# Optimization experiments

Hardware: AMD Instinct MI355X
Metric: run time of the kernel (lower is better)

## Reference

```python
import jax, jax.numpy as jnp
import numpy as np

S, F, H, A, B = 11, 650, 1024, 47, 4096
NEG = -1e9  # stand-in for -inf in masked_fill; softmax weight becomes exactly 0 numerically


def _layernorm(x, g, b):
    m = x.mean(-1, keepdims=True)
    v = ((x - m) ** 2).mean(-1, keepdims=True)
    return (x - m) / jnp.sqrt(v + 1e-5) * g + b


def setup_inputs() -> dict:
    key = jax.random.key(0)
    ks = jax.random.split(key, 16)

    def lin(k, fan_in, fan_out):
        kw, kb = jax.random.split(k)
        s = 1.0 / np.sqrt(fan_in)
        W = jax.random.uniform(kw, (fan_in, fan_out), minval=-s, maxval=s, dtype=jnp.float32)
        b = jax.random.uniform(kb, (fan_out,), minval=-s, maxval=s, dtype=jnp.float32)
        return W, b

    obs = jax.random.normal(ks[0], (B, S, F), dtype=jnp.float32)
    action_mask = jax.random.randint(ks[1], (B, 2, A), 0, 2).astype(jnp.int32)
    action_mask = action_mask.at[:, :, :8].set(1)  # guarantee legal actions per row
    u = jax.random.uniform(ks[2], (B, 2, A), minval=1e-6, maxval=1.0)
    gumbel = -jnp.log(-jnp.log(u))

    W0, b0 = lin(ks[3], S * F, H)
    W1, b1 = lin(ks[4], H, H)
    W2, b2 = lin(ks[5], H, H)
    Wp, bp = lin(ks[6], H, 2 * A)
    Wv, bv = lin(ks[7], H, 1)
    ones = jnp.ones((H,), jnp.float32)
    zeros = jnp.zeros((H,), jnp.float32)
    return {
        'obs': obs, 'action_mask': action_mask, 'gumbel': gumbel,
        'W0': W0, 'b0': b0, 'g0': ones, 'be0': zeros,
        'W1': W1, 'b1': b1, 'g1': ones, 'be1': zeros,
        'W2': W2, 'b2': b2, 'g2': ones, 'be2': zeros,
        'Wp': Wp, 'bp': bp, 'Wv': Wv, 'bv': bv,
    }


def _forward(obs, action_mask, gumbel, W0, b0, g0, be0, W1, b1, g1, be1, W2, b2, g2, be2, Wp, bp, Wv, bv):
    x = obs.reshape(obs.shape[0], -1)
    x = jax.nn.relu(_layernorm(x @ W0 + b0, g0, be0))
    x = jax.nn.relu(_layernorm(x @ W1 + b1, g1, be1))
    x = jax.nn.relu(_layernorm(x @ W2 + b2, g2, be2))  # dropout = eval-mode identity
    policy_logits = (x @ Wp + bp).reshape(-1, 2, A)
    value = (x @ Wv + bv)[:, 0]

    bsz = policy_logits.shape[0]
    rows = jnp.arange(bsz)
    ar = jnp.arange(A)

    # head 1: masked categorical via Gumbel-max
    l1 = jnp.where(action_mask[:, 0, :] == 0, NEG, policy_logits[:, 0, :])
    a1 = jnp.argmax(l1 + gumbel[:, 0, :], axis=-1)
    logp1 = jax.nn.log_softmax(l1, axis=-1)[rows, a1]

    # vectorized mutual-exclusivity mask update (replaces per-batch Python loop)
    m2 = action_mask[:, 1, :]
    oh = ar[None, :] == a1[:, None]
    c_switch = (a1 >= 1) & (a1 <= 6)
    m2 = jnp.where(c_switch[:, None] & oh, 0, m2)
    c_tera = (a1 > 26) & (a1 <= 46)
    rng = (ar >= 27) & (ar < 47)
    m2 = jnp.where(c_tera[:, None] & rng[None, :], 0, m2)
    c_zero = a1 == 0
    col0 = (ar == 0)[None, :]
    m2 = jnp.where(c_zero[:, None] & col0, 0, m2)
    empty = (m2.sum(-1) == 0) & c_zero
    m2 = jnp.where(empty[:, None] & col0, 1, m2)

    l2 = jnp.where(m2 == 0, NEG, policy_logits[:, 1, :])
    a2 = jnp.argmax(l2 + gumbel[:, 1, :], axis=-1)
    logp2 = jax.nn.log_softmax(l2, axis=-1)[rows, a2]

    sampled_actions = jnp.stack([a1, a2], axis=-1)
    policy_log_probs = jnp.stack([logp1, logp2], axis=-1)
    return policy_logits, policy_log_probs, sampled_actions, value


def reference(obs, action_mask, gumbel, W0, b0, g0, be0, W1, b1, g1, be1, W2, b2, g2, be2, Wp, bp, Wv, bv):
    return _forward(obs, action_mask, gumbel, W0, b0, g0, be0, W1, b1, g1, be1, W2, b2, g2, be2, Wp, bp, Wv, bv)
```

## Files before the change

kernel.cpp:

```cpp
#include <hip/hip_runtime.h>
#include <math.h>

#define BATCH 4096
#define HDIM  1024
#define KDIM0 7150
#define KP0   7168
#define KT0   224
#define KTH   32
#define NACT  47
#define NA2   94
#define NEGC  -1000000000.0f

#define LP_OFF  385024
#define ACT_OFF 393216
#define VAL_OFF 401408

typedef _Float16 half8_t  __attribute__((ext_vector_type(8)));
typedef _Float16 half4_t  __attribute__((ext_vector_type(4)));
typedef float    float4_t __attribute__((ext_vector_type(4)));

#define GLOAD16(gp, lp) __builtin_amdgcn_global_load_lds( \
    (__attribute__((address_space(1))) void*)(gp), \
    (__attribute__((address_space(3))) void*)(lp), 16, 0, 0)


__global__ __launch_bounds__(256) void wconv_frag_kernel(
    const float* __restrict__ W, _Float16* __restrict__ Wh,
    _Float16* __restrict__ Wl, int K, int KT)
{
  __shared__ float T[64][65];
  const int k0 = blockIdx.x * 64, n0 = blockIdx.y * 64, t = threadIdx.x;
#pragma unroll
  for (int p = 0; p < 16; ++p) {
    const int idx = p * 256 + t;
    const int r = idx >> 6, c = idx & 63;
    T[r][c] = (k0 + r < K) ? W[(size_t)(k0 + r) * HDIM + n0 + c] : 0.f;
  }
  __syncthreads();
#pragma unroll
  for (int ss = 0; ss < 2; ++ss) {
    const int s    = ss * 256 + t;
    const int tile = s >> 6;
    const int ktl  = tile >> 2, ntl = tile & 3;
    const int lane = s & 63;
    const int quad = lane >> 4, nr = lane & 15;
    half8_t h, l;
#pragma unroll
    for (int j = 0; j < 8; ++j) {
      const float v = T[ktl * 32 + quad * 8 + j][ntl * 16 + nr];
      const _Float16 hh = (_Float16)v;
      h[j] = hh;
      l[j] = (_Float16)((v - (float)hh) * 4096.f);
    }
    const size_t o = ((size_t)((n0 / 16 + ntl) * KT + (k0 / 32 + ktl)) * 64 + lane) * 8;
    *(half8_t*)(Wh + o) = h;
    *(half8_t*)(Wl + o) = l;
  }
}

__global__ __launch_bounds__(512, 4) void gemm_obs_kernel(
    const float* __restrict__ A,
    const _Float16* __restrict__ Wh, const _Float16* __restrict__ Wl,
    float* __restrict__ C, int ktsplit)
{
  __shared__ _Float16 As[2][2][8][512];
  __shared__ _Float16 Ws[2][2][8][512];
  const int f  = blockIdx.x + 8 * (blockIdx.y + 32 * blockIdx.z);
  const int nf = (f & 7) * 64 + (f >> 3);
  const int bx = nf & 7, by = (nf >> 3) & 31, bz = nf >> 8;

  const int t    = threadIdx.x;
  const int lane = t & 63;
  const int w    = t >> 6;
  const int nt0  = bx * 8;
  const int mt0  = by * 8;
  const int ktb  = bz * ktsplit;
  const int nit  = ktsplit;
  const int l15  = lane & 15, quad = lane >> 4;
  const int wmi  = (w >> 2) * 4;
  const int wni  = (w & 3) * 2;

  const float* aRow = A + (size_t)((mt0 + w) * 16 + l15) * KDIM0 + quad * 8;
  const _Float16* wS0 = Wh + (size_t)(nt0 + w) * KT0 * 512 + lane * 8;
  const _Float16* wS1 = Wl + (size_t)(nt0 + w) * KT0 * 512 + lane * 8;

  struct AF8 { float v[8]; };
  auto loadA = [&](int kt) {
    AF8 r;
    const int kg = kt * 32 + quad * 8;
    const float* src = aRow + (size_t)kt * 32;
    if (kg + 8 <= KDIM0) {
#pragma unroll
      for (int c = 0; c < 4; ++c) {
        const float2 p = *(const float2*)(src + c * 2);
        r.v[c * 2] = p.x; r.v[c * 2 + 1] = p.y;
      }
    } else {
#pragma unroll
      for (int j = 0; j < 8; ++j)
        r.v[j] = (kg + j < KDIM0) ? src[j] : 0.f;
    }
    return r;
  };
  auto gw = [&](int kt, int buf) {
    GLOAD16(wS0 + (size_t)kt * 512, &Ws[buf][0][w][0]);
    GLOAD16(wS1 + (size_t)kt * 512, &Ws[buf][1][w][0]);
  };
  auto convst = [&](const AF8& a, int buf) {
    half8_t h, l;
#pragma unroll
    for (int j = 0; j < 8; ++j) {
      const float v = a.v[j];
      const _Float16 hh = (_Float16)v;
      h[j] = hh;
      l[j] = (_Float16)((v - (float)hh) * 4096.f);
    }
    *(half8_t*)&As[buf][0][w][lane * 8] = h;
    *(half8_t*)&As[buf][1][w][lane * 8] = l;
  };

  float4_t acc[4][2], accx[4][2];
#pragma unroll
  for (int i = 0; i < 4; ++i)
#pragma unroll
    for (int j = 0; j < 2; ++j) {
      acc[i][j]  = (float4_t){0.f, 0.f, 0.f, 0.f};
      accx[i][j] = (float4_t){0.f, 0.f, 0.f, 0.f};
    }

  auto mm = [&](int buf) {
    half8_t ah[4], al[4], wh[2], wl[2];
#pragma unroll
    for (int i = 0; i < 4; ++i) {
      ah[i] = *(const half8_t*)&As[buf][0][wmi + i][lane * 8];
      al[i] = *(const half8_t*)&As[buf][1][wmi + i][lane * 8];
    }
#pragma unroll
    for (int j = 0; j < 2; ++j) {
      wh[j] = *(const half8_t*)&Ws[buf][0][wni + j][lane * 8];
      wl[j] = *(const half8_t*)&Ws[buf][1][wni + j][lane * 8];
    }
#pragma unroll
    for (int i = 0; i < 4; ++i)
#pragma unroll
      for (int j = 0; j < 2; ++j) {
        acc[i][j]  = __builtin_amdgcn_mfma_f32_16x16x32_f16(ah[i], wh[j], acc[i][j], 0, 0, 0);
        accx[i][j] = __builtin_amdgcn_mfma_f32_16x16x32_f16(ah[i], wl[j], accx[i][j], 0, 0, 0);
        accx[i][j] = __builtin_amdgcn_mfma_f32_16x16x32_f16(al[i], wh[j], accx[i][j], 0, 0, 0);
      }
  };

  AF8 vaE = loadA(ktb + 0);
  AF8 vaO = loadA(ktb + 1);
  gw(ktb + 0, 0);
  convst(vaE, 0);
  __syncthreads();

  for (int it = 0; it < nit; it += 2) {
    gw(ktb + it + 1, 1);
    convst(vaO, 1);
    if (it + 2 < nit) vaE = loadA(ktb + it + 2);
    mm(0);
    __syncthreads();
    if (it + 2 < nit) { gw(ktb + it + 2, 0); convst(vaE, 0); }
    if (it + 3 < nit) vaO = loadA(ktb + it + 3);
    mm(1);
    __syncthreads();
  }

  float* Cb = C + (size_t)bz * ((size_t)BATCH * HDIM);
  const float sc = 1.0f / 4096.0f;
#pragma unroll
  for (int i = 0; i < 4; ++i) {
    const int row0 = (mt0 + wmi + i) * 16 + quad * 4;
#pragma unroll
    for (int j = 0; j < 2; ++j) {
      const int col = (nt0 + wni + j) * 16 + l15;
      float* cp = Cb + (size_t)row0 * HDIM + col;
#pragma unroll
      for (int r = 0; r < 4; ++r)
        cp[(size_t)r * HDIM] = acc[i][j][r] + accx[i][j][r] * sc;
    }
  }
}

__global__ __launch_bounds__(512, 4) void gemm_frag2_kernel(
    const _Float16* __restrict__ Ah, const _Float16* __restrict__ Al,
    const _Float16* __restrict__ Wh, const _Float16* __restrict__ Wl,
    float* __restrict__ C, int KT, int ktsplit)
{
  __shared__ _Float16 As[2][2][8][512];
  __shared__ _Float16 Ws[2][2][8][512];
  const int f  = blockIdx.x + 8 * (blockIdx.y + 32 * blockIdx.z);
  const int nf = (f & 7) * 64 + (f >> 3);
  const int bx = nf & 7, by = (nf >> 3) & 31, bz = nf >> 8;

  const int t    = threadIdx.x;
  const int lane = t & 63;
  const int w    = t >> 6;
  const int nt0  = bx * 8;
  const int mt0  = by * 8;
  const int ktb  = bz * ktsplit;
  const int nit  = ktsplit;
  const int l15  = lane & 15, quad = lane >> 4;
  const int wmi  = (w >> 2) * 4;
  const int wni  = (w & 3) * 2;

  const _Float16* aS0 = Ah + (size_t)(mt0 + w) * KT * 512 + lane * 8;
  const _Float16* aS1 = Al + (size_t)(mt0 + w) * KT * 512 + lane * 8;
  const _Float16* wS0 = Wh + (size_t)(nt0 + w) * KT * 512 + lane * 8;
  const _Float16* wS1 = Wl + (size_t)(nt0 + w) * KT * 512 + lane * 8;

  auto st = [&](int kt, int buf) {
    GLOAD16(aS0 + (size_t)kt * 512, &As[buf][0][w][0]);
    GLOAD16(aS1 + (size_t)kt * 512, &As[buf][1][w][0]);
    GLOAD16(wS0 + (size_t)kt * 512, &Ws[buf][0][w][0]);
    GLOAD16(wS1 + (size_t)kt * 512, &Ws[buf][1][w][0]);
  };

  float4_t acc[4][2], accx[4][2];
#pragma unroll
  for (int i = 0; i < 4; ++i)
#pragma unroll
    for (int j = 0; j < 2; ++j) {
      acc[i][j]  = (float4_t){0.f, 0.f, 0.f, 0.f};
      accx[i][j] = (float4_t){0.f, 0.f, 0.f, 0.f};
    }

  auto mm = [&](int buf) {
    half8_t ah[4], al[4], wh[2], wl[2];
#pragma unroll
    for (int i = 0; i < 4; ++i) {
      ah[i] = *(const half8_t*)&As[buf][0][wmi + i][lane * 8];
      al[i] = *(const half8_t*)&As[buf][1][wmi + i][lane * 8];
    }
#pragma unroll
    for (int j = 0; j < 2; ++j) {
      wh[j] = *(const half8_t*)&Ws[buf][0][wni + j][lane * 8];
      wl[j] = *(const half8_t*)&Ws[buf][1][wni + j][lane * 8];
    }
#pragma unroll
    for (int i = 0; i < 4; ++i)
#pragma unroll
      for (int j = 0; j < 2; ++j) {
        acc[i][j]  = __builtin_amdgcn_mfma_f32_16x16x32_f16(ah[i], wh[j], acc[i][j], 0, 0, 0);
        accx[i][j] = __builtin_amdgcn_mfma_f32_16x16x32_f16(ah[i], wl[j], accx[i][j], 0, 0, 0);
        accx[i][j] = __builtin_amdgcn_mfma_f32_16x16x32_f16(al[i], wh[j], accx[i][j], 0, 0, 0);
      }
  };

  st(ktb, 0);
  __syncthreads();
  for (int it = 0; it < nit; it += 2) {
    st(ktb + it + 1, 1);
    mm(0);
    __syncthreads();
    if (it + 2 < nit) st(ktb + it + 2, 0);
    mm(1);
    __syncthreads();
  }

  float* Cb = C + (size_t)bz * ((size_t)BATCH * HDIM);
  const float sc = 1.0f / 4096.0f;
#pragma unroll
  for (int i = 0; i < 4; ++i) {
    const int row0 = (mt0 + wmi + i) * 16 + quad * 4;
#pragma unroll
    for (int j = 0; j < 2; ++j) {
      const int col = (nt0 + wni + j) * 16 + l15;
      float* cp = Cb + (size_t)row0 * HDIM + col;
#pragma unroll
      for (int r = 0; r < 4; ++r)
        cp[(size_t)r * HDIM] = acc[i][j][r] + accx[i][j][r] * sc;
    }
  }
}

__global__ __launch_bounds__(1024) void ln_relu_f16_frag_kernel(
    const float* __restrict__ x0, const float* __restrict__ x1,
    const float* __restrict__ bias,
    const float* __restrict__ g, const float* __restrict__ be,
    _Float16* __restrict__ oh, _Float16* __restrict__ ol)
{
  const int t = threadIdx.x;
  const int w = t >> 6, lane = t & 63;
  const int mt = blockIdx.x;
  const float* xr0 = x0 + (size_t)(mt * 16 + w) * HDIM;
  const float* xr1 = x1 + (size_t)(mt * 16 + w) * HDIM;

  float4 v[4];
  float s = 0.f;
#pragma unroll
  for (int c = 0; c < 4; ++c) {
    const int k = c * 256 + lane * 4;
    const float4 a = *(const float4*)(xr0 + k);
    const float4 b = *(const float4*)(xr1 + k);
    const float4 bb = *(const float4*)(bias + k);
    v[c].x = a.x + b.x + bb.x; v[c].y = a.y + b.y + bb.y;
    v[c].z = a.z + b.z + bb.z; v[c].w = a.w + b.w + bb.w;
    s += (v[c].x + v[c].y) + (v[c].z + v[c].w);
  }
#pragma unroll
  for (int o = 32; o; o >>= 1) s += __shfl_xor(s, o, 64);
  const float mean = s * (1.0f / HDIM);

  float s2 = 0.f;
#pragma unroll
  for (int c = 0; c < 4; ++c) {
    v[c].x -= mean; v[c].y -= mean; v[c].z -= mean; v[c].w -= mean;
    s2 += (v[c].x * v[c].x + v[c].y * v[c].y) + (v[c].z * v[c].z + v[c].w * v[c].w);
  }
#pragma unroll
  for (int o = 32; o; o >>= 1) s2 += __shfl_xor(s2, o, 64);
  const float inv = 1.0f / sqrtf(s2 * (1.0f / HDIM) + 1e-5f);

  const int kt_b  = lane >> 3;
  const int quad  = (lane >> 1) & 3;
  const int jb    = (lane & 1) * 4;
#pragma unroll
  for (int c = 0; c < 4; ++c) {
    const int k = c * 256 + lane * 4;
    const float4 gg = *(const float4*)(g + k);
    const float4 ee = *(const float4*)(be + k);
    float r0 = fmaxf(fmaf(v[c].x * inv, gg.x, ee.x), 0.f);
    float r1 = fmaxf(fmaf(v[c].y * inv, gg.y, ee.y), 0.f);
    float r2 = fmaxf(fmaf(v[c].z * inv, gg.z, ee.z), 0.f);
    float r3 = fmaxf(fmaf(v[c].w * inv, gg.w, ee.w), 0.f);
    const _Float16 h0 = (_Float16)r0, h1 = (_Float16)r1, h2 = (_Float16)r2, h3 = (_Float16)r3;
    const half4_t hv = {h0, h1, h2, h3};
    const half4_t lv = {(_Float16)((r0 - (float)h0) * 4096.f),
                        (_Float16)((r1 - (float)h1) * 4096.f),
                        (_Float16)((r2 - (float)h2) * 4096.f),
                        (_Float16)((r3 - (float)h3) * 4096.f)};
    const int kt = c * 8 + kt_b;
    const size_t o = ((size_t)(mt * KTH + kt) * 64 + quad * 16 + w) * 8 + jb;
    *(half4_t*)(oh + o) = hv;
    *(half4_t*)(ol + o) = lv;
  }
}

__global__ __launch_bounds__(256) void pack_wcat_kernel(
    const float* __restrict__ Wp, const float* __restrict__ Wv,
    float* __restrict__ Wc)
{
  const int i = blockIdx.x * 256 + threadIdx.x;
  const int k = i / 96, c = i % 96;
  float v = 0.f;
  if (c < 94)       v = Wp[(size_t)k * 94 + c];
  else if (c == 94) v = Wv[k];
  Wc[i] = v;
}

__global__ __launch_bounds__(256) void head_fused_kernel(
    const float* __restrict__ x0, const float* __restrict__ x1,
    const float* __restrict__ b2, const float* __restrict__ g2,
    const float* __restrict__ be2,
    const float* __restrict__ Wc, const float* __restrict__ bp,
    const float* __restrict__ bv,
    const int* __restrict__ amask, const float* __restrict__ gum,
    float* __restrict__ out)
{
  __shared__ float Xs[8][1025];
  __shared__ float red[4][8][96];
  __shared__ float fl[8][96];
  __shared__ float rstat[16];
  const int t  = threadIdx.x;
  const int r0 = blockIdx.x * 8;
  const int wv = t >> 6, lane = t & 63;

#pragma unroll 4
  for (int i = 0; i < 32; ++i) {
    const int e = i * 256 + t;
    const int r = e >> 10, k = e & 1023;
    const size_t gi = (size_t)(r0 + r) * HDIM + k;
    Xs[r][k] = x0[gi] + x1[gi] + b2[k];
  }
  __syncthreads();

#pragma unroll
  for (int rr = 0; rr < 2; ++rr) {
    const int row = wv + rr * 4;
    float s = 0.f;
#pragma unroll
    for (int ii = 0; ii < 16; ++ii) s += Xs[row][lane + 64 * ii];
#pragma unroll
    for (int o = 32; o; o >>= 1) s += __shfl_xor(s, o, 64);
    const float mean = s * (1.0f / HDIM);
    float s2 = 0.f;
#pragma unroll
    for (int ii = 0; ii < 16; ++ii) {
      const float d = Xs[row][lane + 64 * ii] - mean;
      s2 += d * d;
    }
#pragma unroll
    for (int o = 32; o; o >>= 1) s2 += __shfl_xor(s2, o, 64);
    if (lane == 0) {
      rstat[row] = mean;
      rstat[8 + row] = 1.0f / sqrtf(s2 * (1.0f / HDIM) + 1e-5f);
    }
  }
  __syncthreads();

#pragma unroll 4
  for (int i = 0; i < 32; ++i) {
    const int e = i * 256 + t;
    const int r = e >> 10, k = e & 1023;
    Xs[r][k] = fmaxf(fmaf((Xs[r][k] - rstat[r]) * rstat[8 + r], g2[k], be2[k]), 0.f);
  }
  __syncthreads();

  const int tx = t & 15;
  const int ty = (t >> 4) & 3;
  const int kz = t >> 6;
  const int c0 = tx * 6;
  float acc[2][6] = {{0.f,0.f,0.f,0.f,0.f,0.f},{0.f,0.f,0.f,0.f,0.f,0.f}};
  const int kkend = kz * 256 + 256;
  for (int kk = kz * 256; kk < kkend; ++kk) {
    const float xa = Xs[ty * 2][kk];
    const float xb = Xs[ty * 2 + 1][kk];
    const float* wrow = Wc + (size_t)kk * 96 + c0;
    const float2 w01 = *(const float2*)(wrow);
    const float2 w23 = *(const float2*)(wrow + 2);
    const float2 w45 = *(const float2*)(wrow + 4);
    const float wvv[6] = {w01.x, w01.y, w23.x, w23.y, w45.x, w45.y};
#pragma unroll
    for (int j = 0; j < 6; ++j) {
      acc[0][j] = fmaf(xa, wvv[j], acc[0][j]);
      acc[1][j] = fmaf(xb, wvv[j], acc[1][j]);
    }
  }
#pragma unroll
  for (int r = 0; r < 2; ++r)
#pragma unroll
    for (int j = 0; j < 6; ++j) red[kz][ty * 2 + r][c0 + j] = acc[r][j];
  __syncthreads();

#pragma unroll
  for (int q = 0; q < 3; ++q) {
    const int e = t * 3 + q;
    const int row = e / 96, c = e % 96;
    const float sum = red[0][row][c] + red[1][row][c] + red[2][row][c] + red[3][row][c];
    if (c < 94) {
      const float vv = sum + bp[c];
      out[(size_t)(r0 + row) * NA2 + c] = vv;
      fl[row][c] = vv;
    } else if (c == 94) {
      out[VAL_OFF + r0 + row] = sum + bv[0];
    }
  }
  __syncthreads();

#pragma unroll
  for (int rr = 0; rr < 2; ++rr) {
    const int row = wv + rr * 4;
    const int b = r0 + row;
    const bool valid = lane < NACT;

    const float lg1 = valid ? fl[row][lane] : 0.f;
    const float lg2 = valid ? fl[row][NACT + lane] : 0.f;
    const int   mk1 = valid ? amask[(size_t)b * NA2 + lane] : 0;
    const int   mk2 = valid ? amask[(size_t)b * NA2 + NACT + lane] : 0;
    const float gu1 = valid ? gum[(size_t)b * NA2 + lane] : 0.f;
    const float gu2 = valid ? gum[(size_t)b * NA2 + NACT + lane] : 0.f;

    const float l1 = valid ? ((mk1 == 0) ? NEGC : lg1) : -INFINITY;
    float key = valid ? (l1 + gu1) : -INFINITY;
    int idx = lane;
#pragma unroll
    for (int o = 32; o; o >>= 1) {
      const float ok = __shfl_xor(key, o, 64);
      const int   oi = __shfl_xor(idx, o, 64);
      if (ok > key || (ok == key && oi < idx)) { key = ok; idx = oi; }
    }
    const int a1 = idx;

    float mx = l1;
#pragma unroll
    for (int o = 32; o; o >>= 1) mx = fmaxf(mx, __shfl_xor(mx, o, 64));
    float ex = valid ? expf(l1 - mx) : 0.f;
#pragma unroll
    for (int o = 32; o; o >>= 1) ex += __shfl_xor(ex, o, 64);
    const float logp1 = __shfl(l1, a1, 64) - (mx + logf(ex));

    int m2 = mk2;
    if (a1 >= 1 && a1 <= 6 && lane == a1) m2 = 0;
    if (a1 > 26 && a1 <= 46 && lane >= 27 && valid) m2 = 0;
    if (a1 == 0 && lane == 0) m2 = 0;
    int tot = m2;
#pragma unroll
    for (int o = 32; o; o >>= 1) tot += __shfl_xor(tot, o, 64);
    if (a1 == 0 && tot == 0 && lane == 0) m2 = 1;

    const float l2 = valid ? ((m2 == 0) ? NEGC : lg2) : -INFINITY;
    float key2 = valid ? (l2 + gu2) : -INFINITY;
    int idx2 = lane;
#pragma unroll
    for (int o = 32; o; o >>= 1) {
      const float ok = __shfl_xor(key2, o, 64);
      const int   oi = __shfl_xor(idx2, o, 64);
      if (ok > key2 || (ok == key2 && oi < idx2)) { key2 = ok; idx2 = oi; }
    }
    const int a2 = idx2;

    float mx2 = l2;
#pragma unroll
    for (int o = 32; o; o >>= 1) mx2 = fmaxf(mx2, __shfl_xor(mx2, o, 64));
    float ex2 = valid ? expf(l2 - mx2) : 0.f;
#pragma unroll
    for (int o = 32; o; o >>= 1) ex2 += __shfl_xor(ex2, o, 64);
    const float logp2 = __shfl(l2, a2, 64) - (mx2 + logf(ex2));

    if (lane == 0) {
      out[LP_OFF  + b * 2]     = logp1;
      out[LP_OFF  + b * 2 + 1] = logp2;
      out[ACT_OFF + b * 2]     = (float)a1;
      out[ACT_OFF + b * 2 + 1] = (float)a2;
    }
  }
}

extern "C" void kernel_launch(void* const* d_in, const int* in_sizes, int n_in,
                              void* d_out, int out_size, void* d_ws, size_t ws_size,
                              hipStream_t stream) {
  (void)in_sizes; (void)n_in; (void)out_size; (void)ws_size;
  const float* obs   = (const float*)d_in[0];
  const int*   amask = (const int*)  d_in[1];
  const float* gum   = (const float*)d_in[2];
  const float* W0    = (const float*)d_in[3];
  const float* b0    = (const float*)d_in[4];
  const float* g0    = (const float*)d_in[5];
  const float* be0   = (const float*)d_in[6];
  const float* W1    = (const float*)d_in[7];
  const float* b1    = (const float*)d_in[8];
  const float* g1    = (const float*)d_in[9];
  const float* be1   = (const float*)d_in[10];
  const float* W2    = (const float*)d_in[11];
  const float* b2    = (const float*)d_in[12];
  const float* g2    = (const float*)d_in[13];
  const float* be2   = (const float*)d_in[14];
  const float* Wp    = (const float*)d_in[15];
  const float* bp    = (const float*)d_in[16];
  const float* Wv    = (const float*)d_in[17];
  const float* bv    = (const float*)d_in[18];
  float* out = (float*)d_out;

  char* ws = (char*)d_ws;
  size_t off = 0;
  auto take = [&](size_t n) { char* p = ws + off; off += (n + 255) & ~(size_t)255; return p; };
  _Float16* w0h  = (_Float16*)take((size_t)HDIM * KP0 * 2);
  _Float16* w0l  = (_Float16*)take((size_t)HDIM * KP0 * 2);
  _Float16* w1h  = (_Float16*)take((size_t)HDIM * HDIM * 2);
  _Float16* w1l  = (_Float16*)take((size_t)HDIM * HDIM * 2);
  _Float16* w2h  = (_Float16*)take((size_t)HDIM * HDIM * 2);
  _Float16* w2l  = (_Float16*)take((size_t)HDIM * HDIM * 2);
  float*    xf   = (float*)   take((size_t)2 * BATCH * HDIM * 4);
  float*    wc   = (float*)   take((size_t)HDIM * 96 * 4);
  _Float16* xph  = w0h;
  _Float16* xpl  = w0l;
  float* xf1 = xf + (size_t)BATCH * HDIM;

  wconv_frag_kernel<<<dim3(KP0 / 64, 16), 256, 0, stream>>>(W0, w0h, w0l, KDIM0, KT0);
  wconv_frag_kernel<<<dim3(16, 16), 256, 0, stream>>>(W1, w1h, w1l, HDIM, KTH);
  wconv_frag_kernel<<<dim3(16, 16), 256, 0, stream>>>(W2, w2h, w2l, HDIM, KTH);
  pack_wcat_kernel<<<384, 256, 0, stream>>>(Wp, Wv, wc);

  gemm_obs_kernel<<<dim3(8, 32, 2), 512, 0, stream>>>(obs, w0h, w0l, xf, KT0 / 2);
  ln_relu_f16_frag_kernel<<<BATCH / 16, 1024, 0, stream>>>(xf, xf1, b0, g0, be0, xph, xpl);

  gemm_frag2_kernel<<<dim3(8, 32, 2), 512, 0, stream>>>(xph, xpl, w1h, w1l, xf, KTH, KTH / 2);
  ln_relu_f16_frag_kernel<<<BATCH / 16, 1024, 0, stream>>>(xf, xf1, b1, g1, be1, xph, xpl);

  gemm_frag2_kernel<<<dim3(8, 32, 2), 512, 0, stream>>>(xph, xpl, w2h, w2l, xf, KTH, KTH / 2);

  head_fused_kernel<<<BATCH / 8, 256, 0, stream>>>(
      xf, xf1, b2, g2, be2, wc, bp, bv, amask, gum, out);
}
```

Measured before the change: 530.7 us.

## Triple-buffer weight tiles with explicit vmcnt waits in both GEMM kernels

Both split-K GEMM kernels now give the weight tiles a three-stage LDS ring and prefetch weights two k-steps ahead. The blanket __syncthreads is replaced by a partial s_waitcnt vmcnt(N) plus a barrier, so newer async global-to-LDS loads can stay in flight across iterations. The obs kernel also keeps three register A fragments to prefetch A further ahead. The extra LDS stage may limit occupancy, and the padded trailing iterations issue redundant clamped loads. Correctness depends on the hand-counted vmcnt values matching the real number of outstanding loads.

```diff
diff --git a/kernel.cpp b/kernel.cpp
--- a/kernel.cpp
+++ b/kernel.cpp
@@ -23,6 +23,12 @@
     (__attribute__((address_space(1))) void*)(gp), \
     (__attribute__((address_space(3))) void*)(lp), 16, 0, 0)
 
+#define WBAR_N(N) do { \
+    asm volatile("s_waitcnt vmcnt(" #N ") lgkmcnt(0)" ::: "memory"); \
+    __builtin_amdgcn_s_barrier(); \
+    __builtin_amdgcn_sched_barrier(0); \
+  } while (0)
+
 
 __global__ __launch_bounds__(256) void wconv_frag_kernel(
     const float* __restrict__ W, _Float16* __restrict__ Wh,
@@ -64,7 +70,7 @@
     float* __restrict__ C, int ktsplit)
 {
   __shared__ _Float16 As[2][2][8][512];
-  __shared__ _Float16 Ws[2][2][8][512];
+  __shared__ _Float16 Ws[3][2][8][512];
   const int f  = blockIdx.x + 8 * (blockIdx.y + 32 * blockIdx.z);
   const int nf = (f & 7) * 64 + (f >> 3);
   const int bx = nf & 7, by = (nf >> 3) & 31, bz = nf >> 8;
@@ -76,6 +82,7 @@
   const int mt0  = by * 8;
   const int ktb  = bz * ktsplit;
   const int nit  = ktsplit;
+  const int nitp = ((nit + 2) / 3) * 3;
   const int l15  = lane & 15, quad = lane >> 4;
   const int wmi  = (w >> 2) * 4;
   const int wni  = (w & 3) * 2;
@@ -84,11 +91,15 @@
   const _Float16* wS0 = Wh + (size_t)(nt0 + w) * KT0 * 512 + lane * 8;
   const _Float16* wS1 = Wl + (size_t)(nt0 + w) * KT0 * 512 + lane * 8;
 
+  auto cl2 = [&](int x) { return x < nit ? x : nit - 1; };
+
   struct AF8 { float v[8]; };
-  auto loadA = [&](int kt) {
-    AF8 r;
-    const int kg = kt * 32 + quad * 8;
-    const float* src = aRow + (size_t)kt * 32;
+  AF8 va0, va1, va2;
+
+  auto loadA = [&](int ktl_, AF8& r) {
+    const int ktg = ktb + ktl_;
+    const int kg = ktg * 32 + quad * 8;
+    const float* src = aRow + (size_t)ktg * 32;
     if (kg + 8 <= KDIM0) {
 #pragma unroll
       for (int c = 0; c < 4; ++c) {
@@ -100,13 +111,13 @@
       for (int j = 0; j < 8; ++j)
         r.v[j] = (kg + j < KDIM0) ? src[j] : 0.f;
     }
-    return r;
   };
-  auto gw = [&](int kt, int buf) {
-    GLOAD16(wS0 + (size_t)kt * 512, &Ws[buf][0][w][0]);
-    GLOAD16(wS1 + (size_t)kt * 512, &Ws[buf][1][w][0]);
+  auto gw = [&](int ktl_, int sw) {
+    const size_t kb = (size_t)(ktb + ktl_) * 512;
+    GLOAD16(wS0 + kb, &Ws[sw][0][w][0]);
+    GLOAD16(wS1 + kb, &Ws[sw][1][w][0]);
   };
-  auto convst = [&](const AF8& a, int buf) {
+  auto convst = [&](const AF8& a, int sa) {
     half8_t h, l;
 #pragma unroll
     for (int j = 0; j < 8; ++j) {
@@ -115,8 +126,8 @@
       h[j] = hh;
       l[j] = (_Float16)((v - (float)hh) * 4096.f);
     }
-    *(half8_t*)&As[buf][0][w][lane * 8] = h;
-    *(half8_t*)&As[buf][1][w][lane * 8] = l;
+    *(half8_t*)&As[sa][0][w][lane * 8] = h;
+    *(half8_t*)&As[sa][1][w][lane * 8] = l;
   };
 
   float4_t acc[4][2], accx[4][2];
@@ -128,17 +139,17 @@
       accx[i][j] = (float4_t){0.f, 0.f, 0.f, 0.f};
     }
 
-  auto mm = [&](int buf) {
+  auto mm = [&](int sa, int sw) {
     half8_t ah[4], al[4], wh[2], wl[2];
 #pragma unroll
     for (int i = 0; i < 4; ++i) {
-      ah[i] = *(const half8_t*)&As[buf][0][wmi + i][lane * 8];
-      al[i] = *(const half8_t*)&As[buf][1][wmi + i][lane * 8];
+      ah[i] = *(const half8_t*)&As[sa][0][wmi + i][lane * 8];
+      al[i] = *(const half8_t*)&As[sa][1][wmi + i][lane * 8];
     }
 #pragma unroll
     for (int j = 0; j < 2; ++j) {
-      wh[j] = *(const half8_t*)&Ws[buf][0][wni + j][lane * 8];
-      wl[j] = *(const half8_t*)&Ws[buf][1][wni + j][lane * 8];
+      wh[j] = *(const half8_t*)&Ws[sw][0][wni + j][lane * 8];
+      wl[j] = *(const half8_t*)&Ws[sw][1][wni + j][lane * 8];
     }
 #pragma unroll
     for (int i = 0; i < 4; ++i)
@@ -150,23 +161,32 @@
       }
   };
 
-  AF8 vaE = loadA(ktb + 0);
-  AF8 vaO = loadA(ktb + 1);
-  gw(ktb + 0, 0);
-  convst(vaE, 0);
-  __syncthreads();
-
-  for (int it = 0; it < nit; it += 2) {
-    gw(ktb + it + 1, 1);
-    convst(vaO, 1);
-    if (it + 2 < nit) vaE = loadA(ktb + it + 2);
-    mm(0);
-    __syncthreads();
-    if (it + 2 < nit) { gw(ktb + it + 2, 0); convst(vaE, 0); }
-    if (it + 3 < nit) vaO = loadA(ktb + it + 3);
-    mm(1);
-    __syncthreads();
-  }
+  loadA(cl2(0), va0);
+  __builtin_amdgcn_sched_barrier(0);
+  gw(cl2(0), 0);
+  loadA(cl2(1), va1);
+  __builtin_amdgcn_sched_barrier(0);
+  gw(cl2(1), 1);
+  loadA(cl2(2), va2);
+  convst(va0, 0);
+  WBAR_N(6);
+
+#define OBS_IT(KK, VLD, VCV)                                              \
+  {                                                                       \
+    const int it = itb + (KK);                                            \
+    gw(cl2(it + 2), (it + 2) % 3);                                        \
+    loadA(cl2(it + 3), VLD);                                              \
+    convst(VCV, (it + 1) & 1);                                            \
+    if (it < nit) mm(it & 1, it % 3);                                     \
+    WBAR_N(6);                                                            \
+  }
+
+  for (int itb = 0; itb < nitp; itb += 3) {
+    OBS_IT(0, va0, va1)
+    OBS_IT(1, va1, va2)
+    OBS_IT(2, va2, va0)
+  }
+#undef OBS_IT
 
   float* Cb = C + (size_t)bz * ((size_t)BATCH * HDIM);
   const float sc = 1.0f / 4096.0f;
@@ -190,7 +210,7 @@
     float* __restrict__ C, int KT, int ktsplit)
 {
   __shared__ _Float16 As[2][2][8][512];
-  __shared__ _Float16 Ws[2][2][8][512];
+  __shared__ _Float16 Ws[3][2][8][512];
   const int f  = blockIdx.x + 8 * (blockIdx.y + 32 * blockIdx.z);
   const int nf = (f & 7) * 64 + (f >> 3);
   const int bx = nf & 7, by = (nf >> 3) & 31, bz = nf >> 8;
@@ -202,6 +222,7 @@
   const int mt0  = by * 8;
   const int ktb  = bz * ktsplit;
   const int nit  = ktsplit;
+  const int nitp = nit + 2;
   const int l15  = lane & 15, quad = lane >> 4;
   const int wmi  = (w >> 2) * 4;
   const int wni  = (w & 3) * 2;
@@ -211,11 +232,17 @@
   const _Float16* wS0 = Wh + (size_t)(nt0 + w) * KT * 512 + lane * 8;
   const _Float16* wS1 = Wl + (size_t)(nt0 + w) * KT * 512 + lane * 8;
 
-  auto st = [&](int kt, int buf) {
-    GLOAD16(aS0 + (size_t)kt * 512, &As[buf][0][w][0]);
-    GLOAD16(aS1 + (size_t)kt * 512, &As[buf][1][w][0]);
-    GLOAD16(wS0 + (size_t)kt * 512, &Ws[buf][0][w][0]);
-    GLOAD16(wS1 + (size_t)kt * 512, &Ws[buf][1][w][0]);
+  auto cl2 = [&](int x) { return x < nit ? x : nit - 1; };
+
+  auto ga = [&](int ktl_, int sa) {
+    const size_t kb = (size_t)(ktb + ktl_) * 512;
+    GLOAD16(aS0 + kb, &As[sa][0][w][0]);
+    GLOAD16(aS1 + kb, &As[sa][1][w][0]);
+  };
+  auto gw = [&](int ktl_, int sw) {
+    const size_t kb = (size_t)(ktb + ktl_) * 512;
+    GLOAD16(wS0 + kb, &Ws[sw][0][w][0]);
+    GLOAD16(wS1 + kb, &Ws[sw][1][w][0]);
   };
 
   float4_t acc[4][2], accx[4][2];
@@ -227,17 +254,17 @@
       accx[i][j] = (float4_t){0.f, 0.f, 0.f, 0.f};
     }
 
-  auto mm = [&](int buf) {
+  auto mm = [&](int sa, int sw) {
     half8_t ah[4], al[4], wh[2], wl[2];
 #pragma unroll
     for (int i = 0; i < 4; ++i) {
-      ah[i] = *(const half8_t*)&As[buf][0][wmi + i][lane * 8];
-      al[i] = *(const half8_t*)&As[buf][1][wmi + i][lane * 8];
+      ah[i] = *(const half8_t*)&As[sa][0][wmi + i][lane * 8];
+      al[i] = *(const half8_t*)&As[sa][1][wmi + i][lane * 8];
     }
 #pragma unroll
     for (int j = 0; j < 2; ++j) {
-      wh[j] = *(const half8_t*)&Ws[buf][0][wni + j][lane * 8];
-      wl[j] = *(const half8_t*)&Ws[buf][1][wni + j][lane * 8];
+      wh[j] = *(const half8_t*)&Ws[sw][0][wni + j][lane * 8];
+      wl[j] = *(const half8_t*)&Ws[sw][1][wni + j][lane * 8];
     }
 #pragma unroll
     for (int i = 0; i < 4; ++i)
@@ -249,15 +276,18 @@
       }
   };
 
-  st(ktb, 0);
-  __syncthreads();
-  for (int it = 0; it < nit; it += 2) {
-    st(ktb + it + 1, 1);
-    mm(0);
-    __syncthreads();
-    if (it + 2 < nit) st(ktb + it + 2, 0);
-    mm(1);
-    __syncthreads();
+  ga(cl2(0), 0);
+  gw(cl2(0), 0);
+  __builtin_amdgcn_sched_barrier(0);
+  gw(cl2(1), 1);
+  WBAR_N(2);
+
+  for (int it = 0; it < nitp; ++it) {
+    ga(cl2(it + 1), (it + 1) & 1);
+    __builtin_amdgcn_sched_barrier(0);
+    gw(cl2(it + 2), (it + 2) % 3);
+    if (it < nit) mm(it & 1, it % 3);
+    WBAR_N(2);
   }
 
   float* Cb = C + (size_t)bz * ((size_t)BATCH * HDIM);
```

Result: slower. 545.5 us (+2.8%).
